# Performance work log

Measured on AMD Instinct MI355X. Metric: run time of the kernel, lower is better.

## Reference

```python
import jax, jax.numpy as jnp
import numpy as np

B, T = 8192, 4096
N_GROUPS = 64
SIZES = np.tile(np.array([32, 64, 96, 64], dtype=np.int32), 16)
SEG_IDS = np.repeat(np.arange(N_GROUPS, dtype=np.int32), SIZES)  # [T]


def setup_inputs() -> dict:
    key = jax.random.key(0)
    k1, k2, k3 = jax.random.split(key, 3)
    H = jax.random.normal(k1, (B, T), dtype=jnp.float32)
    # nn.Linear(hidden_dim=1, 1): weight [1,1], bias [1]
    score_w = jax.random.normal(k2, (1, 1), dtype=jnp.float32)
    score_b = jax.random.normal(k3, (1,), dtype=jnp.float32) * 0.1
    return {"H": H, "score_w": score_w, "score_b": score_b}


def reference(H, score_w, score_b):
    seg_ids = jnp.asarray(SEG_IDS)
    sizes = jnp.asarray(SIZES, dtype=H.dtype)  # [G]
    # ragged segment mean over the feature axis: G[b,g] = mean(H[b, sl_g])
    G = jax.ops.segment_sum(H.T, seg_ids, num_segments=N_GROUPS).T / sizes  # [B, G]
    # score = Linear(1,1) applied to G.unsqueeze(-1), then squeeze -> affine on G
    scores = G * score_w[0, 0] + score_b[0]  # [B, G]
    a = jax.nn.softmax(scores, axis=1)  # [B, G]
    Z = jnp.sum(a * G, axis=1)  # [B]
    return Z, a
```

## Files before the change

### kernel.cpp

```cpp
#include <hip/hip_runtime.h>


#define TPB 256

__global__ __launch_bounds__(TPB) void agp_kernel(
    const float* __restrict__ H,
    const float* __restrict__ score_w,
    const float* __restrict__ score_b,
    float* __restrict__ Z,
    float* __restrict__ A,
    int T)
{
  const int b   = blockIdx.x;
  const int tid = threadIdx.x;
  const float4* row = (const float4*)(H + (size_t)b * T);

  __shared__ float partial[4][TPB];

#pragma unroll
  for (int k = 0; k < 4; ++k) {
    float4 v = row[tid + TPB * k];
    partial[k][tid] = (v.x + v.y) + (v.z + v.w);
  }
  __syncthreads();

  if (tid < 64) {
    const int g = tid;
    const int c = g >> 2;
    const int j = g & 3;
    const int k = c >> 2;
    const int w = c & 3;

    const int   start4[4] = {0, 8, 24, 48};
    const int   len4[4]   = {8, 16, 24, 16};
    const float invsz[4]  = {1.f/32.f, 1.f/64.f, 1.f/96.f, 1.f/64.f};

    const float* p = &partial[k][64 * w + start4[j]];
    float s = 0.f;
    const int L = len4[j];
    for (int i = 0; i < L; ++i) s += p[i];

    const float G     = s * invsz[j];
    const float score = G * score_w[0] + score_b[0];

    float m = score;
#pragma unroll
    for (int mask = 32; mask >= 1; mask >>= 1)
      m = fmaxf(m, __shfl_xor(m, mask));

    const float e  = __expf(score - m);
    float se = e;
    float sg = e * G;
#pragma unroll
    for (int mask = 32; mask >= 1; mask >>= 1) {
      se += __shfl_xor(se, mask);
      sg += __shfl_xor(sg, mask);
    }

    A[(size_t)b * 64 + g] = e / se;
    if (g == 0) Z[b] = sg / se;
  }
}

extern "C" void kernel_launch(void* const* d_in, const int* in_sizes, int n_in,
                              void* d_out, int out_size, void* d_ws, size_t ws_size,
                              hipStream_t stream) {
  const float* H  = (const float*)d_in[0];
  const float* sw = (const float*)d_in[1];
  const float* sb = (const float*)d_in[2];

  const int T = 4096;
  const int B = in_sizes[0] / T;

  float* Z = (float*)d_out;
  float* A = Z + B;

  agp_kernel<<<B, TPB, 0, stream>>>(H, sw, sb, Z, A, T);
}
```

Measured before the change: 188.2 us.

## Process one row per wavefront with shuffle-based segment reductions, dropping shared memory

```diff
diff --git a/kernel.cpp b/kernel.cpp
--- a/kernel.cpp
+++ b/kernel.cpp
@@ -8,58 +8,60 @@
     const float* __restrict__ score_w,
     const float* __restrict__ score_b,
     float* __restrict__ Z,
-    float* __restrict__ A,
-    int T)
+    float* __restrict__ A)
 {
-  const int b   = blockIdx.x;
-  const int tid = threadIdx.x;
-  const float4* row = (const float4*)(H + (size_t)b * T);
+  const int lane = threadIdx.x & 63;
+  const int wave = threadIdx.x >> 6;
+  const int row  = blockIdx.x * 4 + wave;
 
-  __shared__ float partial[4][TPB];
+  const float4* row4 = (const float4*)(H + (size_t)row * 4096);
 
+  const int j   = lane & 3;
+  const int myk = lane >> 2;
+
+  const int srcA = (j == 0) ? 0  : (j == 1) ? 8  : (j == 2) ? 24 : 48;
+  const int srcB = (j == 1) ? 16 : (j == 2) ? 32 : 56;
+  const int srcC = 40;
+
+  float acc = 0.f;
 #pragma unroll
-  for (int k = 0; k < 4; ++k) {
-    float4 v = row[tid + TPB * k];
-    partial[k][tid] = (v.x + v.y) + (v.z + v.w);
+  for (int k = 0; k < 16; ++k) {
+    float4 v = row4[64 * k + lane];
+    float s = (v.x + v.y) + (v.z + v.w);
+    s += __shfl_xor(s, 1);
+    s += __shfl_xor(s, 2);
+    s += __shfl_xor(s, 4);
+    float t0 = __shfl(s, srcA);
+    float t1 = __shfl(s, srcB);
+    float t2 = __shfl(s, srcC);
+    float g = t0;
+    if (j >= 1) g += t1;
+    if (j == 2) g += t2;
+    if (k == myk) acc = g;
   }
-  __syncthreads();
 
-  if (tid < 64) {
-    const int g = tid;
-    const int c = g >> 2;
-    const int j = g & 3;
-    const int k = c >> 2;
-    const int w = c & 3;
+  const float invsz = (j == 0) ? (1.f / 32.f)
+                    : (j == 2) ? (1.f / 96.f)
+                               : (1.f / 64.f);
+  const float G     = acc * invsz;
+  const float score = G * score_w[0] + score_b[0];
 
-    const int   start4[4] = {0, 8, 24, 48};
-    const int   len4[4]   = {8, 16, 24, 16};
-    const float invsz[4]  = {1.f/32.f, 1.f/64.f, 1.f/96.f, 1.f/64.f};
+  float m = score;
+#pragma unroll
+  for (int mask = 32; mask >= 1; mask >>= 1)
+    m = fmaxf(m, __shfl_xor(m, mask));
 
-    const float* p = &partial[k][64 * w + start4[j]];
-    float s = 0.f;
-    const int L = len4[j];
-    for (int i = 0; i < L; ++i) s += p[i];
+  const float e = __expf(score - m);
+  float se = e;
+  float sg = e * G;
+#pragma unroll
+  for (int mask = 32; mask >= 1; mask >>= 1) {
+    se += __shfl_xor(se, mask);
+    sg += __shfl_xor(sg, mask);
+  }
 
-    const float G     = s * invsz[j];
-    const float score = G * score_w[0] + score_b[0];
-
-    float m = score;
-#pragma unroll
-    for (int mask = 32; mask >= 1; mask >>= 1)
-      m = fmaxf(m, __shfl_xor(m, mask));
-
-    const float e  = __expf(score - m);
-    float se = e;
-    float sg = e * G;
-#pragma unroll
-    for (int mask = 32; mask >= 1; mask >>= 1) {
-      se += __shfl_xor(se, mask);
-      sg += __shfl_xor(sg, mask);
-    }
-
-    A[(size_t)b * 64 + g] = e / se;
-    if (g == 0) Z[b] = sg / se;
-  }
+  A[(size_t)row * 64 + lane] = e / se;
+  if (lane == 0) Z[row] = sg / se;
 }
 
 extern "C" void kernel_launch(void* const* d_in, const int* in_sizes, int n_in,
@@ -75,5 +77,5 @@
   float* Z = (float*)d_out;
   float* A = Z + B;
 
-  agp_kernel<<<B, TPB, 0, stream>>>(H, sw, sb, Z, A, T);
+  agp_kernel<<<B / 4, TPB, 0, stream>>>(H, sw, sb, Z, A);
 }
```

Measured after the change: 190.1 us. No clear change (+1.0%).
